# Kernel optimization log

Measured on AMD Instinct MI355X. Metric: run time of the kernel, lower is better.

Reference implementation:

```python
import math
import jax, jax.numpy as jnp
import numpy as np

B, S, D, H = 4, 1024, 1024, 16
DK = D // H
NEG = jnp.float32(-1e32)
EPS = 1e-5


def setup_inputs() -> dict:
    key = jax.random.key(0)
    ks = jax.random.split(key, 10)
    s = 1.0 / math.sqrt(D)
    return {
        "query": jax.random.normal(ks[0], (B, S, D), jnp.float32),
        "key": jax.random.normal(ks[1], (B, S, D), jnp.float32),
        "values": jax.random.normal(ks[2], (B, S, D), jnp.float32),
        "lens": jax.random.randint(ks[3], (B,), 0, S).astype(jnp.int32),
        "state_weight": jax.random.normal(ks[4], (1, H, S, S), jnp.float32),
        # params (kq_same=True -> k shares q_linear weights)
        "Wq": jax.random.normal(ks[5], (D, D), jnp.float32) * s,
        "bq": jnp.zeros((D,), jnp.float32),
        "Wv": jax.random.normal(ks[6], (D, D), jnp.float32) * s,
        "bv": jnp.zeros((D,), jnp.float32),
        "Wo": jax.random.normal(ks[7], (D, D), jnp.float32) * s,
        "bo": jnp.zeros((D,), jnp.float32),
        "gamma": jnp.ones((D,), jnp.float32),
        "beta": jnp.zeros((D,), jnp.float32),
    }


def reference(query, key, values, lens, state_weight, Wq, bq, Wv, bv, Wo, bo, gamma, beta):
    # eval-mode forward of DTransformerLayer (peek_cur=False -> strictly causal)
    b, s, d = query.shape
    mask = jnp.tril(jnp.ones((s, s), bool), -1)[None, None]  # [1,1,S,S]

    q = (query @ Wq + bq).reshape(b, s, H, DK).transpose(0, 2, 1, 3)   # bhsd
    k = (key @ Wq + bq).reshape(b, s, H, DK).transpose(0, 2, 1, 3)     # shared weights (kq_same)
    v = (values @ Wv + bv).reshape(b, s, H, DK).transpose(0, 2, 1, 3)

    scores = jnp.einsum('bhqd,bhkd->bhqk', q, k) / math.sqrt(DK)
    scores = jnp.where(mask, scores, NEG)
    scores = jnp.where(mask, scores + state_weight, NEG)
    attn = jax.nn.softmax(scores, axis=-1)
    attn = jnp.where(mask, attn, 0.0)  # fully-masked rows (row 0) -> zeros, matching torch

    ctx = jnp.einsum('bhqk,bhkd->bhqd', attn, v).transpose(0, 2, 1, 3).reshape(b, s, d)
    out = ctx @ Wo + bo

    x = query + out  # dropout is identity in eval
    mu = jnp.mean(x, axis=-1, keepdims=True)
    var = jnp.mean(jnp.square(x - mu), axis=-1, keepdims=True)
    return (x - mu) * jax.lax.rsqrt(var + EPS) * gamma + beta
```

## Files before the change

### kernel.cpp

```cpp
#include <hip/hip_runtime.h>

#define B_ 4
#define S_ 1024
#define D_ 1024
#define H_ 16
#define DK_ 64

typedef __attribute__((ext_vector_type(8))) short short8;
typedef __attribute__((ext_vector_type(4))) float f32x4;
typedef __attribute__((ext_vector_type(16))) float f32x16;

#define CBASE_PACK 0x100C090604020100ULL

static __device__ __forceinline__ unsigned bf16rne(float x) {
    unsigned b = __float_as_uint(x);
    return (b + 0x7FFFu + ((b >> 16) & 1u)) >> 16;
}

__global__ __launch_bounds__(256) void cvt3_bf16(
    const float* __restrict__ q, const float* __restrict__ k,
    const float* __restrict__ v, ushort* __restrict__ out)
{
    const size_t i = ((size_t)blockIdx.x * 256 + threadIdx.x) * 8;
    const size_t FM = (size_t)4 * 1024 * 1024;
    const float* in = (i < FM) ? q : (i < 2 * FM) ? k : v;
    const size_t off = i & (FM - 1);
    const float4 a = *reinterpret_cast<const float4*>(in + off);
    const float4 b = *reinterpret_cast<const float4*>(in + off + 4);
    union { ushort u[8]; int4 vv; } p;
    p.u[0] = (ushort)bf16rne(a.x); p.u[1] = (ushort)bf16rne(a.y);
    p.u[2] = (ushort)bf16rne(a.z); p.u[3] = (ushort)bf16rne(a.w);
    p.u[4] = (ushort)bf16rne(b.x); p.u[5] = (ushort)bf16rne(b.y);
    p.u[6] = (ushort)bf16rne(b.z); p.u[7] = (ushort)bf16rne(b.w);
    *reinterpret_cast<int4*>(out + i) = p.vv;
}

__global__ __launch_bounds__(256) void transpose_cvt3(
    const float* __restrict__ W0, const float* __restrict__ W1,
    const float* __restrict__ W2, ushort* __restrict__ T0,
    ushort* __restrict__ T1, ushort* __restrict__ T2)
{
    __shared__ float ts[32][33];
    const float* W = (blockIdx.z == 0) ? W0 : (blockIdx.z == 1) ? W1 : W2;
    ushort*     Wt = (blockIdx.z == 0) ? T0 : (blockIdx.z == 1) ? T1 : T2;
    const int t  = threadIdx.x;
    const int k0 = blockIdx.y * 32, n0 = blockIdx.x * 32;
    const int r  = t >> 3, c4 = (t & 7) * 4;
    const float4 v = *reinterpret_cast<const float4*>(&W[(size_t)(k0 + r) * 1024 + n0 + c4]);
    ts[r][c4] = v.x; ts[r][c4 + 1] = v.y; ts[r][c4 + 2] = v.z; ts[r][c4 + 3] = v.w;
    __syncthreads();
    ushort4 o;
    o.x = (ushort)bf16rne(ts[c4    ][r]);
    o.y = (ushort)bf16rne(ts[c4 + 1][r]);
    o.z = (ushort)bf16rne(ts[c4 + 2][r]);
    o.w = (ushort)bf16rne(ts[c4 + 3][r]);
    *reinterpret_cast<ushort4*>(&Wt[(size_t)(n0 + r) * 1024 + k0 + c4]) = o;
}

template<int MODE>
__global__ __launch_bounds__(256) void gemm_mfma(
    const ushort* __restrict__ X, const ushort* __restrict__ Wt,
    const float* __restrict__ bias, const float* __restrict__ resid,
    void* __restrict__ out0, void* __restrict__ out1)
{
    __shared__ ushort As[2][64 * 64];
    __shared__ ushort Bs[2][128 * 64];

    const int t    = threadIdx.x;
    const int lane = t & 63;
    const int w    = t >> 6;

    const int cpx     = gridDim.x >> 3;
    const int logical = (blockIdx.x & 7) * cpx + (blockIdx.x >> 3);
    const int bm = logical >> 3;
    const int bn = logical & 7;

    const int srow   = lane >> 3;
    const int schunk = (lane & 7) ^ srow;
    const ushort* ag[2];
    const ushort* bg[4];
#pragma unroll
    for (int j = 0; j < 2; ++j)
        ag[j] = X  + (size_t)(bm * 64 + (j * 4 + w) * 8 + srow) * 1024 + schunk * 8;
#pragma unroll
    for (int j = 0; j < 4; ++j)
        bg[j] = Wt + (size_t)(bn * 128 + (j * 4 + w) * 8 + srow) * 1024 + schunk * 8;

#define STAGE(buf, k0)                                                           \
    do {                                                                         \
        _Pragma("unroll")                                                        \
        for (int j = 0; j < 2; ++j)                                              \
            __builtin_amdgcn_global_load_lds(                                    \
                (__attribute__((address_space(1))) const void*)(ag[j] + (k0)),   \
                (__attribute__((address_space(3))) void*)&As[buf][(j * 4 + w) * 512], \
                16, 0, 0);                                                       \
        _Pragma("unroll")                                                        \
        for (int j = 0; j < 4; ++j)                                              \
            __builtin_amdgcn_global_load_lds(                                    \
                (__attribute__((address_space(1))) const void*)(bg[j] + (k0)),   \
                (__attribute__((address_space(3))) void*)&Bs[buf][(j * 4 + w) * 512], \
                16, 0, 0);                                                       \
    } while (0)

    const int fr = lane & 15;
    const int fk = lane >> 4;
    const int wm = w >> 1, wn = w & 1;

    f32x4 acc[2][4];
#pragma unroll
    for (int m = 0; m < 2; ++m)
#pragma unroll
        for (int n = 0; n < 4; ++n) acc[m][n] = (f32x4){0.f, 0.f, 0.f, 0.f};

    STAGE(0, 0);
#pragma unroll 1
    for (int kt = 0; kt < 16; ++kt) {
        const int cur = kt & 1;
        if (kt + 1 < 16) {
            STAGE(cur ^ 1, (kt + 1) * 64);
            asm volatile("s_waitcnt vmcnt(6)" ::: "memory");
        } else {
            asm volatile("s_waitcnt vmcnt(0)" ::: "memory");
        }
        __builtin_amdgcn_s_barrier();
        __builtin_amdgcn_sched_barrier(0);
#pragma unroll
        for (int ks = 0; ks < 2; ++ks) {
            short8 af[2], bf[4];
#pragma unroll
            for (int m = 0; m < 2; ++m) {
                const int row = wm * 32 + m * 16 + fr;
                af[m] = *reinterpret_cast<const short8*>(
                    &As[cur][row * 64 + (((ks * 4 + fk) ^ (row & 7)) * 8)]);
            }
#pragma unroll
            for (int n = 0; n < 4; ++n) {
                const int row = wn * 64 + n * 16 + fr;
                bf[n] = *reinterpret_cast<const short8*>(
                    &Bs[cur][row * 64 + (((ks * 4 + fk) ^ (row & 7)) * 8)]);
            }
            __builtin_amdgcn_s_setprio(1);
#pragma unroll
            for (int m = 0; m < 2; ++m)
#pragma unroll
                for (int n = 0; n < 4; ++n)
                    acc[m][n] = __builtin_amdgcn_mfma_f32_16x16x32_bf16(
                        af[m], bf[n], acc[m][n], 0, 0, 0);
            __builtin_amdgcn_s_setprio(0);
        }
        __builtin_amdgcn_sched_barrier(0);
        __builtin_amdgcn_s_barrier();
        __builtin_amdgcn_sched_barrier(0);
    }
#undef STAGE

#pragma unroll
    for (int m = 0; m < 2; ++m) {
        const int row0 = bm * 64 + wm * 32 + m * 16 + fk * 4;
#pragma unroll
        for (int n = 0; n < 4; ++n) {
            const int col = bn * 128 + wn * 64 + n * 16 + fr;
            const float bc = bias[col];
            if (MODE == 0) {
                float* o = (float*)out0;
#pragma unroll
                for (int j = 0; j < 4; ++j) {
                    const int row = row0 + j;
                    o[(size_t)row * 1024 + col] =
                        acc[m][n][j] + bc + resid[(size_t)row * 1024 + col];
                }
            } else if (MODE == 1) {
                ushort* o = (row0 < 4096) ? (ushort*)out0 : (ushort*)out1;
                const int r0 = row0 & 4095;
                const int b_ = r0 >> 10, s0 = r0 & 1023;
                const int h  = col >> 6,  dk = col & 63;
#pragma unroll
                for (int j = 0; j < 4; ++j)
                    o[(((size_t)b_ * H_ + h) * S_ + s0 + j) * DK_ + dk] =
                        (ushort)bf16rne(acc[m][n][j] + bc);
            } else {
                ushort* o = (ushort*)out0;
                const int b_ = row0 >> 10, s0 = row0 & 1023;
                const int h  = col >> 6,   dk = col & 63;
                ushort4 pk;
                pk.x = (ushort)bf16rne(acc[m][n][0] + bc);
                pk.y = (ushort)bf16rne(acc[m][n][1] + bc);
                pk.z = (ushort)bf16rne(acc[m][n][2] + bc);
                pk.w = (ushort)bf16rne(acc[m][n][3] + bc);
                *reinterpret_cast<ushort4*>(
                    &o[(((size_t)b_ * H_ + h) * DK_ + dk) * S_ + s0]) = pk;
            }
        }
    }
}

__global__ __launch_bounds__(256) void attn_mfma(
    const ushort* __restrict__ Qh, const ushort* __restrict__ Kh,
    const ushort* __restrict__ Vt, const float* __restrict__ SW,
    ushort* __restrict__ ctxP, float2* __restrict__ ml)
{
    __shared__ ushort Ks[2][4096];
    __shared__ ushort Vs[2][4096];

    const int t    = threadIdx.x;
    const int lane = t & 63;
    const int w    = t >> 6;
    const int lg = (blockIdx.x & 7) * 160 + (blockIdx.x >> 3);
    const int bh = lg / 20;
    const int ci = lg - bh * 20;
    const int b  = bh >> 4;
    const int h  = bh & 15;
    int qb = 0;
#pragma unroll
    for (int q = 1; q < 8; ++q)
        if ((int)((CBASE_PACK >> (q * 8)) & 0xff) <= ci) qb = q;
    const int lc = ci - (int)((CBASE_PACK >> (qb * 8)) & 0xff);
    const int t0 = lc * 4;
    const int nt = min(4, 2 * qb + 2 - t0);

    const int ql = lane & 31;
    const int hi = lane >> 5;
    const int qrow = qb * 128 + ql * 4 + w;

    const ushort* Kg  = Kh + (size_t)bh * S_ * DK_;
    const ushort* Vg  = Vt + (size_t)bh * DK_ * S_;
    const float*  swp = SW + ((size_t)h * S_ + qrow) * S_;

    const ushort* kgp[2];
    const ushort* vgp[2];
#pragma unroll
    for (int j = 0; j < 2; ++j) {
        const int bb = w * 2 + j;
        const int g = bb >> 2, c = bb & 3;
        kgp[j] = Kg + (size_t)(g * 32 + ql) * DK_ + c * 16 + hi * 8;
        vgp[j] = Vg + (size_t)(g * 32 + ql) * S_  + c * 16 + hi * 8;
    }

#define ASTAGE(buf, k0)                                                          \
    do {                                                                         \
        _Pragma("unroll")                                                        \
        for (int j = 0; j < 2; ++j) {                                            \
            const int bb = w * 2 + j;                                            \
            __builtin_amdgcn_global_load_lds(                                    \
                (__attribute__((address_space(1))) const void*)(kgp[j] + (size_t)(k0) * DK_), \
                (__attribute__((address_space(3))) void*)&Ks[buf][bb * 512],     \
                16, 0, 0);                                                       \
            __builtin_amdgcn_global_load_lds(                                    \
                (__attribute__((address_space(1))) const void*)(vgp[j] + (k0)),  \
                (__attribute__((address_space(3))) void*)&Vs[buf][bb * 512],     \
                16, 0, 0);                                                       \
        }                                                                        \
    } while (0)

    short8 qf[4];
    {
        const ushort* Qg = Qh + ((size_t)bh * S_ + qrow) * DK_;
#pragma unroll
        for (int c = 0; c < 4; ++c) {
            union { int4 i; short8 s; } u;
            u.i = *reinterpret_cast<const int4*>(&Qg[c * 16 + hi * 8]);
            qf[c] = u.s;
        }
    }

    f32x16 accA, accB;
#pragma unroll
    for (int r = 0; r < 16; ++r) { accA[r] = 0.f; accB[r] = 0.f; }
    float mrow = -1e30f, lrow = 0.f;

    ASTAGE(0, t0 * 64);

#pragma unroll 1
    for (int kt = 0; kt < nt; ++kt) {
        const int cur = kt & 1;
        const int k0  = (t0 + kt) * 64;
        if (kt + 1 < nt) {
            ASTAGE(cur ^ 1, (t0 + kt + 1) * 64);
            asm volatile("s_waitcnt vmcnt(4)" ::: "memory");
        } else {
            asm volatile("s_waitcnt vmcnt(0)" ::: "memory");
        }
        __builtin_amdgcn_s_barrier();
        __builtin_amdgcn_sched_barrier(0);

        f32x16 sc[2];
        __builtin_amdgcn_s_setprio(1);
#pragma unroll
        for (int g = 0; g < 2; ++g) {
#pragma unroll
            for (int r = 0; r < 16; ++r) sc[g][r] = 0.f;
#pragma unroll
            for (int c = 0; c < 4; ++c) {
                const short8 kf = *reinterpret_cast<const short8*>(
                    &Ks[cur][((g * 4 + c) * 64 + lane) * 8]);
                sc[g] = __builtin_amdgcn_mfma_f32_32x32x16_bf16(kf, qf[c], sc[g], 0, 0, 0);
            }
        }
        __builtin_amdgcn_s_setprio(0);

        float swv[2][16];
#pragma unroll
        for (int g = 0; g < 2; ++g)
#pragma unroll
            for (int j = 0; j < 4; ++j) {
                const float4 v = *reinterpret_cast<const float4*>(
                    &swp[k0 + g * 32 + hi * 4 + j * 8]);
                swv[g][j * 4 + 0] = v.x; swv[g][j * 4 + 1] = v.y;
                swv[g][j * 4 + 2] = v.z; swv[g][j * 4 + 3] = v.w;
            }

        float pr[2][16];
        float tmax = -1e30f;
        if (t0 + kt >= 2 * qb) {
#pragma unroll
            for (int g = 0; g < 2; ++g)
#pragma unroll
                for (int r = 0; r < 16; ++r) {
                    const int key = k0 + g * 32 + (r & 3) + ((r >> 2) << 3) + (hi << 2);
                    const float s = (key < qrow) ? sc[g][r] * 0.125f + swv[g][r] : -1e30f;
                    pr[g][r] = s;
                    tmax = fmaxf(tmax, s);
                }
        } else {
#pragma unroll
            for (int g = 0; g < 2; ++g)
#pragma unroll
                for (int r = 0; r < 16; ++r) {
                    const float s = sc[g][r] * 0.125f + swv[g][r];
                    pr[g][r] = s;
                    tmax = fmaxf(tmax, s);
                }
        }
        tmax = fmaxf(tmax, __shfl_xor(tmax, 32, 64));
        const float mnew = fmaxf(mrow, tmax);
        const float corr = __expf(mrow - mnew);
        float psum = 0.f;
#pragma unroll
        for (int g = 0; g < 2; ++g)
#pragma unroll
            for (int r = 0; r < 16; ++r) {
                const float e = (pr[g][r] > -1e29f) ? __expf(pr[g][r] - mnew) : 0.f;
                pr[g][r] = e;
                psum += e;
            }
        psum += __shfl_xor(psum, 32, 64);
        lrow = lrow * corr + psum;
        mrow = mnew;
#pragma unroll
        for (int r = 0; r < 16; ++r) { accA[r] *= corr; accB[r] *= corr; }

        short8 paf[4];
#pragma unroll
        for (int g = 0; g < 2; ++g) {
            unsigned pk[8];
#pragma unroll
            for (int j = 0; j < 8; ++j) {
                unsigned r_;
                asm("v_cvt_pk_bf16_f32 %0, %1, %2"
                    : "=v"(r_) : "v"(pr[g][2 * j]), "v"(pr[g][2 * j + 1]));
                pk[j] = r_;
            }
            unsigned x0 = (unsigned)__shfl_xor((int)pk[0], 32, 64);
            unsigned x1 = (unsigned)__shfl_xor((int)pk[1], 32, 64);
            unsigned x2 = (unsigned)__shfl_xor((int)pk[2], 32, 64);
            unsigned x3 = (unsigned)__shfl_xor((int)pk[3], 32, 64);
            unsigned x4 = (unsigned)__shfl_xor((int)pk[4], 32, 64);
            unsigned x5 = (unsigned)__shfl_xor((int)pk[5], 32, 64);
            unsigned x6 = (unsigned)__shfl_xor((int)pk[6], 32, 64);
            unsigned x7 = (unsigned)__shfl_xor((int)pk[7], 32, 64);
            union { unsigned u[4]; short8 s; } a0, a1;
            a0.u[0] = hi ? x2 : pk[0];
            a0.u[1] = hi ? x3 : pk[1];
            a0.u[2] = hi ? pk[2] : x0;
            a0.u[3] = hi ? pk[3] : x1;
            a1.u[0] = hi ? x6 : pk[4];
            a1.u[1] = hi ? x7 : pk[5];
            a1.u[2] = hi ? pk[6] : x4;
            a1.u[3] = hi ? pk[7] : x5;
            paf[g * 2 + 0] = a0.s;
            paf[g * 2 + 1] = a1.s;
        }

        __builtin_amdgcn_s_setprio(1);
#pragma unroll
        for (int cc = 0; cc < 4; ++cc) {
            const short8 va = *reinterpret_cast<const short8*>(
                &Vs[cur][((0 * 4 + cc) * 64 + lane) * 8]);
            const short8 vb = *reinterpret_cast<const short8*>(
                &Vs[cur][((1 * 4 + cc) * 64 + lane) * 8]);
            accA = __builtin_amdgcn_mfma_f32_32x32x16_bf16(va, paf[cc], accA, 0, 0, 0);
            accB = __builtin_amdgcn_mfma_f32_32x32x16_bf16(vb, paf[cc], accB, 0, 0, 0);
        }
        __builtin_amdgcn_s_setprio(0);

        __builtin_amdgcn_sched_barrier(0);
        __builtin_amdgcn_s_barrier();
        __builtin_amdgcn_sched_barrier(0);
    }
#undef ASTAGE

    const float inv = (lrow > 0.f) ? 1.f / lrow : 0.f;
    ushort* crow_ = ctxP + ((size_t)(bh * 20 + ci) * 128 + (ql * 4 + w)) * 64;
#pragma unroll
    for (int g = 0; g < 4; ++g) {
        ushort4 oA, oB;
        oA.x = (ushort)bf16rne(accA[4 * g + 0] * inv);
        oA.y = (ushort)bf16rne(accA[4 * g + 1] * inv);
        oA.z = (ushort)bf16rne(accA[4 * g + 2] * inv);
        oA.w = (ushort)bf16rne(accA[4 * g + 3] * inv);
        oB.x = (ushort)bf16rne(accB[4 * g + 0] * inv);
        oB.y = (ushort)bf16rne(accB[4 * g + 1] * inv);
        oB.z = (ushort)bf16rne(accB[4 * g + 2] * inv);
        oB.w = (ushort)bf16rne(accB[4 * g + 3] * inv);
        *reinterpret_cast<ushort4*>(&crow_[g * 8 + hi * 4])      = oA;
        *reinterpret_cast<ushort4*>(&crow_[g * 8 + hi * 4 + 32]) = oB;
    }
    if (hi == 0) {
        float2 v; v.x = mrow; v.y = lrow;
        ml[(size_t)(bh * 20 + ci) * 128 + ql * 4 + w] = v;
    }
}

__global__ __launch_bounds__(256) void attn_merge(
    const ushort* __restrict__ ctxP, const float2* __restrict__ ml,
    ushort* __restrict__ ctx)
{
    const size_t idx = ((size_t)blockIdx.x * 256 + threadIdx.x) * 8;
    const int col = (int)(idx & 1023);
    const int row = (int)(idx >> 10);
    const int b = row >> 10, s = row & 1023;
    const int h = col >> 6, dk0 = col & 63;
    const int bh = b * 16 + h;
    const int qb = s >> 7, rl = s & 127;
    const int nch = (qb + 2) >> 1;
    const int cb  = (int)((CBASE_PACK >> (qb * 8)) & 0xff);

    float mm[4], ll[4];
    float m = -1e30f;
#pragma unroll
    for (int c = 0; c < 4; ++c)
        if (c < nch) {
            const float2 v = ml[(size_t)(bh * 20 + cb + c) * 128 + rl];
            mm[c] = v.x; ll[c] = v.y;
            m = fmaxf(m, v.x);
        }
    float wc[4], wsum = 0.f;
#pragma unroll
    for (int c = 0; c < 4; ++c)
        if (c < nch) { wc[c] = ll[c] * __expf(mm[c] - m); wsum += wc[c]; }
    const float inv = (wsum > 0.f) ? 1.f / wsum : 0.f;

    float o[8] = {0.f, 0.f, 0.f, 0.f, 0.f, 0.f, 0.f, 0.f};
#pragma unroll
    for (int c = 0; c < 4; ++c)
        if (c < nch) {
            union { int4 v; ushort u[8]; } p;
            p.v = *reinterpret_cast<const int4*>(
                &ctxP[((size_t)(bh * 20 + cb + c) * 128 + rl) * 64 + dk0]);
            const float wgt = wc[c] * inv;
#pragma unroll
            for (int i = 0; i < 8; ++i)
                o[i] += wgt * __uint_as_float((unsigned)p.u[i] << 16);
        }
    union { int4 v; ushort u[8]; } r;
#pragma unroll
    for (int i = 0; i < 8; ++i) r.u[i] = (ushort)bf16rne(o[i]);
    *reinterpret_cast<int4*>(ctx + idx) = r.v;
}

__global__ __launch_bounds__(256) void layernorm_k(
    const float* __restrict__ x, const float* __restrict__ gamma,
    const float* __restrict__ beta, float* __restrict__ out)
{
    const int row = blockIdx.x;
    const int t   = threadIdx.x;
    const float4 v = *reinterpret_cast<const float4*>(&x[(size_t)row * D_ + (t << 2)]);
    float sum = v.x + v.y + v.z + v.w;
    float sq  = v.x * v.x + v.y * v.y + v.z * v.z + v.w * v.w;
#pragma unroll
    for (int w = 1; w < 64; w <<= 1) {
        sum += __shfl_xor(sum, w, 64);
        sq  += __shfl_xor(sq,  w, 64);
    }
    __shared__ float red[8];
    const int wid = t >> 6;
    if ((t & 63) == 0) { red[wid] = sum; red[wid + 4] = sq; }
    __syncthreads();
    sum = red[0] + red[1] + red[2] + red[3];
    sq  = red[4] + red[5] + red[6] + red[7];
    const float mu  = sum * (1.f / 1024.f);
    const float var = sq * (1.f / 1024.f) - mu * mu;
    const float rs  = rsqrtf(var + 1e-5f);
    const float4 gm = *reinterpret_cast<const float4*>(&gamma[t << 2]);
    const float4 bt = *reinterpret_cast<const float4*>(&beta[t << 2]);
    float4 o;
    o.x = (v.x - mu) * rs * gm.x + bt.x;
    o.y = (v.y - mu) * rs * gm.y + bt.y;
    o.z = (v.z - mu) * rs * gm.z + bt.z;
    o.w = (v.w - mu) * rs * gm.w + bt.w;
    *reinterpret_cast<float4*>(&out[(size_t)row * D_ + (t << 2)]) = o;
}

extern "C" void kernel_launch(void* const* d_in, const int* in_sizes, int n_in,
                              void* d_out, int out_size, void* d_ws, size_t ws_size,
                              hipStream_t stream)
{
    const float* query  = (const float*)d_in[0];
    const float* key    = (const float*)d_in[1];
    const float* values = (const float*)d_in[2];
    const float* SW     = (const float*)d_in[4];
    const float* Wq     = (const float*)d_in[5];
    const float* bq     = (const float*)d_in[6];
    const float* Wv     = (const float*)d_in[7];
    const float* bv     = (const float*)d_in[8];
    const float* Wo     = (const float*)d_in[9];
    const float* bo     = (const float*)d_in[10];
    const float* gamma  = (const float*)d_in[11];
    const float* beta   = (const float*)d_in[12];

    char* ws = (char*)d_ws;
    const size_t MB = 1024 * 1024;
    ushort* Qh   = (ushort*)(ws);
    ushort* Kh   = (ushort*)(ws +  8 * MB);
    ushort* Vt   = (ushort*)(ws + 16 * MB);
    ushort* Wqt  = (ushort*)(ws + 24 * MB);
    ushort* Wvt  = (ushort*)(ws + 26 * MB);
    ushort* Wot  = (ushort*)(ws + 28 * MB);
    ushort* qbf  = (ushort*)(ws + 30 * MB);
    ushort* kbf  = (ushort*)(ws + 38 * MB);
    ushort* vbf  = (ushort*)(ws + 46 * MB);
    float2* ml   = (float2*)(ws + 54 * MB);
    ushort* ctxP = qbf;
    ushort* ctxm = Qh;
    float*  xbf  = (float*)(ws + 8 * MB);

    const dim3 blk(256);

    cvt3_bf16<<<dim3(6144), blk, 0, stream>>>(query, key, values, qbf);
    transpose_cvt3<<<dim3(32, 32, 3), blk, 0, stream>>>(Wq, Wv, Wo, Wqt, Wvt, Wot);

    gemm_mfma<1><<<dim3(1024), blk, 0, stream>>>(qbf, Wqt, bq, nullptr, Qh, Kh);
    gemm_mfma<2><<<dim3(512),  blk, 0, stream>>>(vbf, Wvt, bv, nullptr, Vt, nullptr);

    attn_mfma<<<dim3(1280), blk, 0, stream>>>(Qh, Kh, Vt, SW, ctxP, ml);
    attn_merge<<<dim3(2048), blk, 0, stream>>>(ctxP, ml, ctxm);

    gemm_mfma<0><<<dim3(512), blk, 0, stream>>>(ctxm, Wot, bo, query, xbf, nullptr);

    layernorm_k<<<dim3(4096), blk, 0, stream>>>(xbf, gamma, beta, (float*)d_out);
}
```

Baseline: 148.1 us.

## Prefetch state_weight tiles in registers, fold Q scaling into projection, remap blocks

Moves the state_weight loads out of the softmax critical path by double-buffering them in registers one tile ahead, alongside the existing K/V LDS staging. The loop is unrolled by two so buffer indices are static. The 1/sqrt(dk) scale is folded into the Q projection epilogue, and the unmasked exp path drops its mask compare. The block-to-(b,h,chunk) mapping now interleaves batches so concurrent blocks share state_weight rows in cache, and launch bounds request 3 blocks per CU. The register prefetch raises VGPR pressure. The unrolled loop assumes an even tile count nt, and runs tile kt+1 even when nt is odd.

Result: slower. 234.4 us (+58.3%).

```diff
diff --git a/kernel.cpp b/kernel.cpp
--- a/kernel.cpp
+++ b/kernel.cpp
@@ -171,13 +171,14 @@
                 }
             } else if (MODE == 1) {
                 ushort* o = (row0 < 4096) ? (ushort*)out0 : (ushort*)out1;
+                const float qs = (row0 < 4096) ? 0.125f : 1.0f;
                 const int r0 = row0 & 4095;
                 const int b_ = r0 >> 10, s0 = r0 & 1023;
                 const int h  = col >> 6,  dk = col & 63;
 #pragma unroll
                 for (int j = 0; j < 4; ++j)
                     o[(((size_t)b_ * H_ + h) * S_ + s0 + j) * DK_ + dk] =
-                        (ushort)bf16rne(acc[m][n][j] + bc);
+                        (ushort)bf16rne((acc[m][n][j] + bc) * qs);
             } else {
                 ushort* o = (ushort*)out0;
                 const int b_ = row0 >> 10, s0 = row0 & 1023;
@@ -194,7 +195,7 @@
     }
 }
 
-__global__ __launch_bounds__(256) void attn_mfma(
+__global__ __launch_bounds__(256, 3) void attn_mfma(
     const ushort* __restrict__ Qh, const ushort* __restrict__ Kh,
     const ushort* __restrict__ Vt, const float* __restrict__ SW,
     ushort* __restrict__ ctxP, float2* __restrict__ ml)
@@ -206,10 +207,11 @@
     const int lane = t & 63;
     const int w    = t >> 6;
     const int lg = (blockIdx.x & 7) * 160 + (blockIdx.x >> 3);
-    const int bh = lg / 20;
-    const int ci = lg - bh * 20;
-    const int b  = bh >> 4;
-    const int h  = bh & 15;
+    const int b  = lg & 3;
+    const int hc = lg >> 2;
+    const int h  = hc / 20;
+    const int ci = hc % 20;
+    const int bh = b * 16 + h;
     int qb = 0;
 #pragma unroll
     for (int q = 1; q < 8; ++q)
@@ -252,6 +254,16 @@
         }                                                                        \
     } while (0)
 
+#define SWLOAD(dst, k0)                                                          \
+    do {                                                                         \
+        _Pragma("unroll")                                                        \
+        for (int g2 = 0; g2 < 2; ++g2)                                           \
+            _Pragma("unroll")                                                    \
+            for (int j2 = 0; j2 < 4; ++j2)                                       \
+                dst[g2 * 4 + j2] = *reinterpret_cast<const float4*>(             \
+                    &swp[(k0) + g2 * 32 + hi * 4 + j2 * 8]);                     \
+    } while (0)
+
     short8 qf[4];
     {
         const ushort* Qg = Qh + ((size_t)bh * S_ + qrow) * DK_;
@@ -268,18 +280,10 @@
     for (int r = 0; r < 16; ++r) { accA[r] = 0.f; accB[r] = 0.f; }
     float mrow = -1e30f, lrow = 0.f;
 
-    ASTAGE(0, t0 * 64);
-
-#pragma unroll 1
-    for (int kt = 0; kt < nt; ++kt) {
-        const int cur = kt & 1;
-        const int k0  = (t0 + kt) * 64;
-        if (kt + 1 < nt) {
-            ASTAGE(cur ^ 1, (t0 + kt + 1) * 64);
-            asm volatile("s_waitcnt vmcnt(4)" ::: "memory");
-        } else {
-            asm volatile("s_waitcnt vmcnt(0)" ::: "memory");
-        }
+    float4 swA[8], swB[8];
+
+    auto tile_body = [&](int ktt, int cur, const float4 (&swc)[8]) {
+        const int k0 = (t0 + ktt) * 64;
         __builtin_amdgcn_s_barrier();
         __builtin_amdgcn_sched_barrier(0);
 
@@ -298,27 +302,17 @@
         }
         __builtin_amdgcn_s_setprio(0);
 
-        float swv[2][16];
-#pragma unroll
-        for (int g = 0; g < 2; ++g)
-#pragma unroll
-            for (int j = 0; j < 4; ++j) {
-                const float4 v = *reinterpret_cast<const float4*>(
-                    &swp[k0 + g * 32 + hi * 4 + j * 8]);
-                swv[g][j * 4 + 0] = v.x; swv[g][j * 4 + 1] = v.y;
-                swv[g][j * 4 + 2] = v.z; swv[g][j * 4 + 3] = v.w;
-            }
-
-        float pr[2][16];
+        const bool masked = (t0 + ktt >= 2 * qb);
         float tmax = -1e30f;
-        if (t0 + kt >= 2 * qb) {
+        if (masked) {
 #pragma unroll
             for (int g = 0; g < 2; ++g)
 #pragma unroll
                 for (int r = 0; r < 16; ++r) {
                     const int key = k0 + g * 32 + (r & 3) + ((r >> 2) << 3) + (hi << 2);
-                    const float s = (key < qrow) ? sc[g][r] * 0.125f + swv[g][r] : -1e30f;
-                    pr[g][r] = s;
+                    const float swv = ((const float*)&swc[g * 4 + (r >> 2)])[r & 3];
+                    const float s = (key < qrow) ? sc[g][r] + swv : -1e30f;
+                    sc[g][r] = s;
                     tmax = fmaxf(tmax, s);
                 }
         } else {
@@ -326,8 +320,9 @@
             for (int g = 0; g < 2; ++g)
 #pragma unroll
                 for (int r = 0; r < 16; ++r) {
-                    const float s = sc[g][r] * 0.125f + swv[g][r];
-                    pr[g][r] = s;
+                    const float swv = ((const float*)&swc[g * 4 + (r >> 2)])[r & 3];
+                    const float s = sc[g][r] + swv;
+                    sc[g][r] = s;
                     tmax = fmaxf(tmax, s);
                 }
         }
@@ -335,14 +330,25 @@
         const float mnew = fmaxf(mrow, tmax);
         const float corr = __expf(mrow - mnew);
         float psum = 0.f;
-#pragma unroll
-        for (int g = 0; g < 2; ++g)
-#pragma unroll
-            for (int r = 0; r < 16; ++r) {
-                const float e = (pr[g][r] > -1e29f) ? __expf(pr[g][r] - mnew) : 0.f;
-                pr[g][r] = e;
-                psum += e;
-            }
+        if (masked) {
+#pragma unroll
+            for (int g = 0; g < 2; ++g)
+#pragma unroll
+                for (int r = 0; r < 16; ++r) {
+                    const float e = (sc[g][r] > -1e29f) ? __expf(sc[g][r] - mnew) : 0.f;
+                    sc[g][r] = e;
+                    psum += e;
+                }
+        } else {
+#pragma unroll
+            for (int g = 0; g < 2; ++g)
+#pragma unroll
+                for (int r = 0; r < 16; ++r) {
+                    const float e = __expf(sc[g][r] - mnew);
+                    sc[g][r] = e;
+                    psum += e;
+                }
+        }
         psum += __shfl_xor(psum, 32, 64);
         lrow = lrow * corr + psum;
         mrow = mnew;
@@ -357,7 +363,7 @@
             for (int j = 0; j < 8; ++j) {
                 unsigned r_;
                 asm("v_cvt_pk_bf16_f32 %0, %1, %2"
-                    : "=v"(r_) : "v"(pr[g][2 * j]), "v"(pr[g][2 * j + 1]));
+                    : "=v"(r_) : "v"(sc[g][2 * j]), "v"(sc[g][2 * j + 1]));
                 pk[j] = r_;
             }
             unsigned x0 = (unsigned)__shfl_xor((int)pk[0], 32, 64);
@@ -396,8 +402,29 @@
         __builtin_amdgcn_sched_barrier(0);
         __builtin_amdgcn_s_barrier();
         __builtin_amdgcn_sched_barrier(0);
+    };
+
+    SWLOAD(swA, t0 * 64);
+    ASTAGE(0, t0 * 64);
+
+#pragma unroll 1
+    for (int kt = 0; kt < nt; kt += 2) {
+        SWLOAD(swB, (t0 + kt + 1) * 64);
+        ASTAGE(1, (t0 + kt + 1) * 64);
+        asm volatile("s_waitcnt vmcnt(12)" ::: "memory");
+        tile_body(kt, 0, swA);
+
+        if (kt + 2 < nt) {
+            SWLOAD(swA, (t0 + kt + 2) * 64);
+            ASTAGE(0, (t0 + kt + 2) * 64);
+            asm volatile("s_waitcnt vmcnt(12)" ::: "memory");
+        } else {
+            asm volatile("s_waitcnt vmcnt(0)" ::: "memory");
+        }
+        tile_body(kt + 1, 1, swB);
     }
 #undef ASTAGE
+#undef SWLOAD
 
     const float inv = (lrow > 0.f) ? 1.f / lrow : 0.f;
     ushort* crow_ = ctxP + ((size_t)(bh * 20 + ci) * 128 + (ql * 4 + w)) * 64;
```

## Drop LDS staging in attention, load K/V to registers, fold scale and bias

Applied to the files above, without the earlier changes.

The attention kernel no longer double-buffers K/V tiles through shared memory with block barriers. Each wave now loads its K and V fragments straight from global memory into registers and prefetches the next K tile and state_weight tile. The 1/sqrt(dk) scale moves into the Q projection epilogue, and state_weight seeds the score MFMA accumulator, removing the per-element scale and add. Block indexing is remapped so the four batches sharing a head's state_weight rows run next to each other, aiming for better L2 reuse. In exchange, all four waves now fetch the same K/V fragments separately, which multiplies global/L2 traffic and raises register pressure.

Result: slower. 165.9 us (+12.0%).

```diff
diff --git a/kernel.cpp b/kernel.cpp
--- a/kernel.cpp
+++ b/kernel.cpp
@@ -171,13 +171,14 @@
                 }
             } else if (MODE == 1) {
                 ushort* o = (row0 < 4096) ? (ushort*)out0 : (ushort*)out1;
+                const float qs = (row0 < 4096) ? 0.125f : 1.0f;
                 const int r0 = row0 & 4095;
                 const int b_ = r0 >> 10, s0 = r0 & 1023;
                 const int h  = col >> 6,  dk = col & 63;
 #pragma unroll
                 for (int j = 0; j < 4; ++j)
                     o[(((size_t)b_ * H_ + h) * S_ + s0 + j) * DK_ + dk] =
-                        (ushort)bf16rne(acc[m][n][j] + bc);
+                        (ushort)bf16rne((acc[m][n][j] + bc) * qs);
             } else {
                 ushort* o = (ushort*)out0;
                 const int b_ = row0 >> 10, s0 = row0 & 1023;
@@ -199,17 +200,15 @@
     const ushort* __restrict__ Vt, const float* __restrict__ SW,
     ushort* __restrict__ ctxP, float2* __restrict__ ml)
 {
-    __shared__ ushort Ks[2][4096];
-    __shared__ ushort Vs[2][4096];
-
     const int t    = threadIdx.x;
     const int lane = t & 63;
     const int w    = t >> 6;
     const int lg = (blockIdx.x & 7) * 160 + (blockIdx.x >> 3);
-    const int bh = lg / 20;
-    const int ci = lg - bh * 20;
-    const int b  = bh >> 4;
-    const int h  = bh & 15;
+    const int b  = lg & 3;
+    const int hc = lg >> 2;
+    const int h  = hc / 20;
+    const int ci = hc % 20;
+    const int bh = b * 16 + h;
     int qb = 0;
 #pragma unroll
     for (int q = 1; q < 8; ++q)
@@ -226,32 +225,6 @@
     const ushort* Vg  = Vt + (size_t)bh * DK_ * S_;
     const float*  swp = SW + ((size_t)h * S_ + qrow) * S_;
 
-    const ushort* kgp[2];
-    const ushort* vgp[2];
-#pragma unroll
-    for (int j = 0; j < 2; ++j) {
-        const int bb = w * 2 + j;
-        const int g = bb >> 2, c = bb & 3;
-        kgp[j] = Kg + (size_t)(g * 32 + ql) * DK_ + c * 16 + hi * 8;
-        vgp[j] = Vg + (size_t)(g * 32 + ql) * S_  + c * 16 + hi * 8;
-    }
-
-#define ASTAGE(buf, k0)                                                          \
-    do {                                                                         \
-        _Pragma("unroll")                                                        \
-        for (int j = 0; j < 2; ++j) {                                            \
-            const int bb = w * 2 + j;                                            \
-            __builtin_amdgcn_global_load_lds(                                    \
-                (__attribute__((address_space(1))) const void*)(kgp[j] + (size_t)(k0) * DK_), \
-                (__attribute__((address_space(3))) void*)&Ks[buf][bb * 512],     \
-                16, 0, 0);                                                       \
-            __builtin_amdgcn_global_load_lds(                                    \
-                (__attribute__((address_space(1))) const void*)(vgp[j] + (k0)),  \
-                (__attribute__((address_space(3))) void*)&Vs[buf][bb * 512],     \
-                16, 0, 0);                                                       \
-        }                                                                        \
-    } while (0)
-
     short8 qf[4];
     {
         const ushort* Qg = Qh + ((size_t)bh * S_ + qrow) * DK_;
@@ -268,136 +241,142 @@
     for (int r = 0; r < 16; ++r) { accA[r] = 0.f; accB[r] = 0.f; }
     float mrow = -1e30f, lrow = 0.f;
 
-    ASTAGE(0, t0 * 64);
-
+    int4 kA[8];
+    int4 vv[8];
+    float4 sA[8], sB[8];
+
+#define LOADK(kt_)                                                               \
+    do {                                                                         \
+        const size_t kb_ = (size_t)(t0 + (kt_)) * 64 * DK_;                      \
+        _Pragma("unroll")                                                        \
+        for (int j = 0; j < 8; ++j)                                              \
+            kA[j] = *reinterpret_cast<const int4*>(                              \
+                &Kg[kb_ + (size_t)((j >> 2) * 32 + ql) * DK_ + (j & 3) * 16 + hi * 8]); \
+    } while (0)
+
+#define LOADV(kt_)                                                               \
+    do {                                                                         \
+        const int kv_ = (t0 + (kt_)) * 64;                                       \
+        _Pragma("unroll")                                                        \
+        for (int j = 0; j < 8; ++j)                                              \
+            vv[j] = *reinterpret_cast<const int4*>(                              \
+                &Vg[(size_t)((j >> 2) * 32 + ql) * S_ + kv_ + (j & 3) * 16 + hi * 8]); \
+    } while (0)
+
+#define LOADS(dst, kt_)                                                          \
+    do {                                                                         \
+        const int ks_ = (t0 + (kt_)) * 64;                                       \
+        _Pragma("unroll")                                                        \
+        for (int j = 0; j < 8; ++j)                                              \
+            dst[j] = *reinterpret_cast<const float4*>(                           \
+                &swp[ks_ + (j >> 2) * 32 + hi * 4 + (j & 3) * 8]);               \
+    } while (0)
+
+#define BODY(CURS, NXTS, ktt)                                                    \
+    do {                                                                         \
+        const int k0_ = (t0 + (ktt)) * 64;                                       \
+        LOADV(ktt);                                                              \
+                            \
+        f32x16 sc0, sc1;                                                         \
+        _Pragma("unroll")                                                        \
+        for (int r = 0; r < 16; ++r) {                                           \
+            sc0[r] = ((const float*)&CURS[(r >> 2)])[r & 3];                     \
+            sc1[r] = ((const float*)&CURS[4 + (r >> 2)])[r & 3];                 \
+        }                                                                        \
+        _Pragma("unroll")                                                        \
+        for (int c = 0; c < 4; ++c) {                                            \
+            union { int4 i; short8 s; } k0u, k1u;                                \
+            k0u.i = kA[c];  k1u.i = kA[4 + c];                                   \
+            sc0 = __builtin_amdgcn_mfma_f32_32x32x16_bf16(k0u.s, qf[c], sc0, 0, 0, 0); \
+            sc1 = __builtin_amdgcn_mfma_f32_32x32x16_bf16(k1u.s, qf[c], sc1, 0, 0, 0); \
+        }                                                                        \
+                           \
+        if ((ktt) + 1 < nt) { LOADK((ktt) + 1); LOADS(NXTS, (ktt) + 1); }        \
+                                \
+        float tmax = -1e30f;                                                     \
+        if (t0 + (ktt) >= 2 * qb) {                                              \
+            _Pragma("unroll")                                                    \
+            for (int r = 0; r < 16; ++r) {                                       \
+                const int key0 = k0_ + (r & 3) + ((r >> 2) << 3) + (hi << 2);    \
+                if (key0 >= qrow)      sc0[r] = -1e30f;                          \
+                if (key0 + 32 >= qrow) sc1[r] = -1e30f;                          \
+                tmax = fmaxf(tmax, fmaxf(sc0[r], sc1[r]));                       \
+            }                                                                    \
+        } else {                                                                 \
+            _Pragma("unroll")                                                    \
+            for (int r = 0; r < 16; ++r)                                         \
+                tmax = fmaxf(tmax, fmaxf(sc0[r], sc1[r]));                       \
+        }                                                                        \
+        tmax = fmaxf(tmax, __shfl_xor(tmax, 32, 64));                            \
+        const float mnew = fmaxf(mrow, tmax);                                    \
+        const float corr = __expf(mrow - mnew);                                  \
+        float psum = 0.f;                                                        \
+        _Pragma("unroll")                                                        \
+        for (int r = 0; r < 16; ++r) {                                           \
+            const float e0 = (sc0[r] > -1e29f) ? __expf(sc0[r] - mnew) : 0.f;    \
+            const float e1 = (sc1[r] > -1e29f) ? __expf(sc1[r] - mnew) : 0.f;    \
+            sc0[r] = e0; sc1[r] = e1;                                            \
+            psum += e0 + e1;                                                     \
+        }                                                                        \
+        psum += __shfl_xor(psum, 32, 64);                                        \
+        lrow = lrow * corr + psum;                                               \
+        mrow = mnew;                                                             \
+        _Pragma("unroll")                                                        \
+        for (int r = 0; r < 16; ++r) { accA[r] *= corr; accB[r] *= corr; }       \
+                       \
+        short8 paf[4];                                                           \
+        _Pragma("unroll")                                                        \
+        for (int g = 0; g < 2; ++g) {                                            \
+            unsigned pk[8];                                                      \
+            _Pragma("unroll")                                                    \
+            for (int j = 0; j < 8; ++j) {                                        \
+                unsigned r_;                                                     \
+                const float lo_ = g ? sc1[2 * j]     : sc0[2 * j];               \
+                const float hi_ = g ? sc1[2 * j + 1] : sc0[2 * j + 1];           \
+                asm("v_cvt_pk_bf16_f32 %0, %1, %2" : "=v"(r_) : "v"(lo_), "v"(hi_)); \
+                pk[j] = r_;                                                      \
+            }                                                                    \
+            unsigned x0 = (unsigned)__shfl_xor((int)pk[0], 32, 64);              \
+            unsigned x1 = (unsigned)__shfl_xor((int)pk[1], 32, 64);              \
+            unsigned x2 = (unsigned)__shfl_xor((int)pk[2], 32, 64);              \
+            unsigned x3 = (unsigned)__shfl_xor((int)pk[3], 32, 64);              \
+            unsigned x4 = (unsigned)__shfl_xor((int)pk[4], 32, 64);              \
+            unsigned x5 = (unsigned)__shfl_xor((int)pk[5], 32, 64);              \
+            unsigned x6 = (unsigned)__shfl_xor((int)pk[6], 32, 64);              \
+            unsigned x7 = (unsigned)__shfl_xor((int)pk[7], 32, 64);              \
+            union { unsigned u[4]; short8 s; } a0, a1;                           \
+            a0.u[0] = hi ? x2 : pk[0];                                           \
+            a0.u[1] = hi ? x3 : pk[1];                                           \
+            a0.u[2] = hi ? pk[2] : x0;                                           \
+            a0.u[3] = hi ? pk[3] : x1;                                           \
+            a1.u[0] = hi ? x6 : pk[4];                                           \
+            a1.u[1] = hi ? x7 : pk[5];                                           \
+            a1.u[2] = hi ? pk[6] : x4;                                           \
+            a1.u[3] = hi ? pk[7] : x5;                                           \
+            paf[g * 2 + 0] = a0.s;                                               \
+            paf[g * 2 + 1] = a1.s;                                               \
+        }                                                                        \
+                                             \
+        _Pragma("unroll")                                                        \
+        for (int cc = 0; cc < 4; ++cc) {                                         \
+            union { int4 i; short8 s; } va, vb;                                  \
+            va.i = vv[cc]; vb.i = vv[4 + cc];                                    \
+            accA = __builtin_amdgcn_mfma_f32_32x32x16_bf16(va.s, paf[cc], accA, 0, 0, 0); \
+            accB = __builtin_amdgcn_mfma_f32_32x32x16_bf16(vb.s, paf[cc], accB, 0, 0, 0); \
+        }                                                                        \
+    } while (0)
+
+    LOADK(0);
+    LOADS(sA, 0);
 #pragma unroll 1
-    for (int kt = 0; kt < nt; ++kt) {
-        const int cur = kt & 1;
-        const int k0  = (t0 + kt) * 64;
-        if (kt + 1 < nt) {
-            ASTAGE(cur ^ 1, (t0 + kt + 1) * 64);
-            asm volatile("s_waitcnt vmcnt(4)" ::: "memory");
-        } else {
-            asm volatile("s_waitcnt vmcnt(0)" ::: "memory");
-        }
-        __builtin_amdgcn_s_barrier();
-        __builtin_amdgcn_sched_barrier(0);
-
-        f32x16 sc[2];
-        __builtin_amdgcn_s_setprio(1);
-#pragma unroll
-        for (int g = 0; g < 2; ++g) {
-#pragma unroll
-            for (int r = 0; r < 16; ++r) sc[g][r] = 0.f;
-#pragma unroll
-            for (int c = 0; c < 4; ++c) {
-                const short8 kf = *reinterpret_cast<const short8*>(
-                    &Ks[cur][((g * 4 + c) * 64 + lane) * 8]);
-                sc[g] = __builtin_amdgcn_mfma_f32_32x32x16_bf16(kf, qf[c], sc[g], 0, 0, 0);
-            }
-        }
-        __builtin_amdgcn_s_setprio(0);
-
-        float swv[2][16];
-#pragma unroll
-        for (int g = 0; g < 2; ++g)
-#pragma unroll
-            for (int j = 0; j < 4; ++j) {
-                const float4 v = *reinterpret_cast<const float4*>(
-                    &swp[k0 + g * 32 + hi * 4 + j * 8]);
-                swv[g][j * 4 + 0] = v.x; swv[g][j * 4 + 1] = v.y;
-                swv[g][j * 4 + 2] = v.z; swv[g][j * 4 + 3] = v.w;
-            }
-
-        float pr[2][16];
-        float tmax = -1e30f;
-        if (t0 + kt >= 2 * qb) {
-#pragma unroll
-            for (int g = 0; g < 2; ++g)
-#pragma unroll
-                for (int r = 0; r < 16; ++r) {
-                    const int key = k0 + g * 32 + (r & 3) + ((r >> 2) << 3) + (hi << 2);
-                    const float s = (key < qrow) ? sc[g][r] * 0.125f + swv[g][r] : -1e30f;
-                    pr[g][r] = s;
-                    tmax = fmaxf(tmax, s);
-                }
-        } else {
-#pragma unroll
-            for (int g = 0; g < 2; ++g)
-#pragma unroll
-                for (int r = 0; r < 16; ++r) {
-                    const float s = sc[g][r] * 0.125f + swv[g][r];
-                    pr[g][r] = s;
-                    tmax = fmaxf(tmax, s);
-                }
-        }
-        tmax = fmaxf(tmax, __shfl_xor(tmax, 32, 64));
-        const float mnew = fmaxf(mrow, tmax);
-        const float corr = __expf(mrow - mnew);
-        float psum = 0.f;
-#pragma unroll
-        for (int g = 0; g < 2; ++g)
-#pragma unroll
-            for (int r = 0; r < 16; ++r) {
-                const float e = (pr[g][r] > -1e29f) ? __expf(pr[g][r] - mnew) : 0.f;
-                pr[g][r] = e;
-                psum += e;
-            }
-        psum += __shfl_xor(psum, 32, 64);
-        lrow = lrow * corr + psum;
-        mrow = mnew;
-#pragma unroll
-        for (int r = 0; r < 16; ++r) { accA[r] *= corr; accB[r] *= corr; }
-
-        short8 paf[4];
-#pragma unroll
-        for (int g = 0; g < 2; ++g) {
-            unsigned pk[8];
-#pragma unroll
-            for (int j = 0; j < 8; ++j) {
-                unsigned r_;
-                asm("v_cvt_pk_bf16_f32 %0, %1, %2"
-                    : "=v"(r_) : "v"(pr[g][2 * j]), "v"(pr[g][2 * j + 1]));
-                pk[j] = r_;
-            }
-            unsigned x0 = (unsigned)__shfl_xor((int)pk[0], 32, 64);
-            unsigned x1 = (unsigned)__shfl_xor((int)pk[1], 32, 64);
-            unsigned x2 = (unsigned)__shfl_xor((int)pk[2], 32, 64);
-            unsigned x3 = (unsigned)__shfl_xor((int)pk[3], 32, 64);
-            unsigned x4 = (unsigned)__shfl_xor((int)pk[4], 32, 64);
-            unsigned x5 = (unsigned)__shfl_xor((int)pk[5], 32, 64);
-            unsigned x6 = (unsigned)__shfl_xor((int)pk[6], 32, 64);
-            unsigned x7 = (unsigned)__shfl_xor((int)pk[7], 32, 64);
-            union { unsigned u[4]; short8 s; } a0, a1;
-            a0.u[0] = hi ? x2 : pk[0];
-            a0.u[1] = hi ? x3 : pk[1];
-            a0.u[2] = hi ? pk[2] : x0;
-            a0.u[3] = hi ? pk[3] : x1;
-            a1.u[0] = hi ? x6 : pk[4];
-            a1.u[1] = hi ? x7 : pk[5];
-            a1.u[2] = hi ? pk[6] : x4;
-            a1.u[3] = hi ? pk[7] : x5;
-            paf[g * 2 + 0] = a0.s;
-            paf[g * 2 + 1] = a1.s;
-        }
-
-        __builtin_amdgcn_s_setprio(1);
-#pragma unroll
-        for (int cc = 0; cc < 4; ++cc) {
-            const short8 va = *reinterpret_cast<const short8*>(
-                &Vs[cur][((0 * 4 + cc) * 64 + lane) * 8]);
-            const short8 vb = *reinterpret_cast<const short8*>(
-                &Vs[cur][((1 * 4 + cc) * 64 + lane) * 8]);
-            accA = __builtin_amdgcn_mfma_f32_32x32x16_bf16(va, paf[cc], accA, 0, 0, 0);
-            accB = __builtin_amdgcn_mfma_f32_32x32x16_bf16(vb, paf[cc], accB, 0, 0, 0);
-        }
-        __builtin_amdgcn_s_setprio(0);
-
-        __builtin_amdgcn_sched_barrier(0);
-        __builtin_amdgcn_s_barrier();
-        __builtin_amdgcn_sched_barrier(0);
-    }
-#undef ASTAGE
+    for (int kt = 0; kt < nt; kt += 2) {
+        BODY(sA, sB, kt);
+        BODY(sB, sA, kt + 1);
+    }
+#undef LOADK
+#undef LOADV
+#undef LOADS
+#undef BODY
 
     const float inv = (lrow > 0.f) ? 1.f / lrow : 0.f;
     ushort* crow_ = ctxP + ((size_t)(bh * 20 + ci) * 128 + (ql * 4 + w)) * 64;
```

## Fuse fp32-to-bf16 input conversion into projection GEMMs and fold score scale into Q

Applied to the files above, without the earlier changes.

Removes the separate cvt3_bf16 pass. The projection GEMMs now load fp32 activations into registers, convert them with v_cvt_pk_bf16_f32 and write bf16 to LDS, while B still goes through direct global-to-LDS loads. The 1/sqrt(dk) scale is applied to Q in the GEMM epilogue, so the attention kernel no longer multiplies scores. The attention kernel also reorders its block-to-(batch, head) mapping and issues the state_weight loads before the QK MFMAs to hide their latency. The cost is that the GEMM A loads go through registers with a conversion step, which adds register pressure and waitcnt bookkeeping in the main loop.

New measurement: 145.0 us. 2.1% less time.

```diff
diff --git a/kernel.cpp b/kernel.cpp
--- a/kernel.cpp
+++ b/kernel.cpp
@@ -15,24 +15,6 @@
 static __device__ __forceinline__ unsigned bf16rne(float x) {
     unsigned b = __float_as_uint(x);
     return (b + 0x7FFFu + ((b >> 16) & 1u)) >> 16;
-}
-
-__global__ __launch_bounds__(256) void cvt3_bf16(
-    const float* __restrict__ q, const float* __restrict__ k,
-    const float* __restrict__ v, ushort* __restrict__ out)
-{
-    const size_t i = ((size_t)blockIdx.x * 256 + threadIdx.x) * 8;
-    const size_t FM = (size_t)4 * 1024 * 1024;
-    const float* in = (i < FM) ? q : (i < 2 * FM) ? k : v;
-    const size_t off = i & (FM - 1);
-    const float4 a = *reinterpret_cast<const float4*>(in + off);
-    const float4 b = *reinterpret_cast<const float4*>(in + off + 4);
-    union { ushort u[8]; int4 vv; } p;
-    p.u[0] = (ushort)bf16rne(a.x); p.u[1] = (ushort)bf16rne(a.y);
-    p.u[2] = (ushort)bf16rne(a.z); p.u[3] = (ushort)bf16rne(a.w);
-    p.u[4] = (ushort)bf16rne(b.x); p.u[5] = (ushort)bf16rne(b.y);
-    p.u[6] = (ushort)bf16rne(b.z); p.u[7] = (ushort)bf16rne(b.w);
-    *reinterpret_cast<int4*>(out + i) = p.vv;
 }
 
 __global__ __launch_bounds__(256) void transpose_cvt3(
@@ -58,10 +40,175 @@
 }
 
 template<int MODE>
-__global__ __launch_bounds__(256) void gemm_mfma(
+__global__ __launch_bounds__(256) void gemm_f32a(
+    const float* __restrict__ Xf0, const float* __restrict__ Xf1,
+    const ushort* __restrict__ Wt, const float* __restrict__ bias,
+    void* __restrict__ out0, void* __restrict__ out1)
+{
+    __shared__ ushort As[2][64 * 64];
+    __shared__ ushort Bs[2][128 * 64];
+
+    const int t    = threadIdx.x;
+    const int lane = t & 63;
+    const int w    = t >> 6;
+
+    const int cpx     = gridDim.x >> 3;
+    const int logical = (blockIdx.x & 7) * cpx + (blockIdx.x >> 3);
+    const int bm = logical >> 3;
+    const int bn = logical & 7;
+
+    const int srow   = lane >> 3;
+    const int schunk = (lane & 7) ^ srow;
+
+    const float* Xf = (MODE == 1 && bm >= 64) ? Xf1 : Xf0;
+    const int rbase = (bm * 64) & 4095;
+    const float* ap[2];
+#pragma unroll
+    for (int j = 0; j < 2; ++j)
+        ap[j] = Xf + (size_t)(rbase + (j * 4 + w) * 8 + srow) * 1024 + schunk * 8;
+
+    const ushort* bg[4];
+#pragma unroll
+    for (int j = 0; j < 4; ++j)
+        bg[j] = Wt + (size_t)(bn * 128 + (j * 4 + w) * 8 + srow) * 1024 + schunk * 8;
+
+    float4 aRx0, aRy0, aRx1, aRy1;
+
+#define A_ISSUE(k0)                                                              \
+    do {                                                                         \
+        aRx0 = *reinterpret_cast<const float4*>(ap[0] + (k0));                   \
+        aRy0 = *reinterpret_cast<const float4*>(ap[0] + (k0) + 4);               \
+        aRx1 = *reinterpret_cast<const float4*>(ap[1] + (k0));                   \
+        aRy1 = *reinterpret_cast<const float4*>(ap[1] + (k0) + 4);               \
+    } while (0)
+
+#define B_STAGE(buf, k0)                                                         \
+    do {                                                                         \
+        _Pragma("unroll")                                                        \
+        for (int j = 0; j < 4; ++j)                                              \
+            __builtin_amdgcn_global_load_lds(                                    \
+                (__attribute__((address_space(1))) const void*)(bg[j] + (k0)),   \
+                (__attribute__((address_space(3))) void*)&Bs[buf][(j * 4 + w) * 512], \
+                16, 0, 0);                                                       \
+    } while (0)
+
+#define A_WRITE(buf)                                                             \
+    do {                                                                         \
+        union { unsigned u[4]; int4 v; } p0, p1;                                 \
+        asm("v_cvt_pk_bf16_f32 %0, %1, %2" : "=v"(p0.u[0]) : "v"(aRx0.x), "v"(aRx0.y)); \
+        asm("v_cvt_pk_bf16_f32 %0, %1, %2" : "=v"(p0.u[1]) : "v"(aRx0.z), "v"(aRx0.w)); \
+        asm("v_cvt_pk_bf16_f32 %0, %1, %2" : "=v"(p0.u[2]) : "v"(aRy0.x), "v"(aRy0.y)); \
+        asm("v_cvt_pk_bf16_f32 %0, %1, %2" : "=v"(p0.u[3]) : "v"(aRy0.z), "v"(aRy0.w)); \
+        asm("v_cvt_pk_bf16_f32 %0, %1, %2" : "=v"(p1.u[0]) : "v"(aRx1.x), "v"(aRx1.y)); \
+        asm("v_cvt_pk_bf16_f32 %0, %1, %2" : "=v"(p1.u[1]) : "v"(aRx1.z), "v"(aRx1.w)); \
+        asm("v_cvt_pk_bf16_f32 %0, %1, %2" : "=v"(p1.u[2]) : "v"(aRy1.x), "v"(aRy1.y)); \
+        asm("v_cvt_pk_bf16_f32 %0, %1, %2" : "=v"(p1.u[3]) : "v"(aRy1.z), "v"(aRy1.w)); \
+        *reinterpret_cast<int4*>(&As[buf][((0 * 4 + w) * 64 + lane) * 8]) = p0.v; \
+        *reinterpret_cast<int4*>(&As[buf][((1 * 4 + w) * 64 + lane) * 8]) = p1.v; \
+    } while (0)
+
+    const int fr = lane & 15;
+    const int fk = lane >> 4;
+    const int wm = w >> 1, wn = w & 1;
+
+    f32x4 acc[2][4];
+#pragma unroll
+    for (int m = 0; m < 2; ++m)
+#pragma unroll
+        for (int n = 0; n < 4; ++n) acc[m][n] = (f32x4){0.f, 0.f, 0.f, 0.f};
+
+    A_ISSUE(0);
+    B_STAGE(0, 0);
+    asm volatile("s_waitcnt vmcnt(4)" ::: "memory");
+    A_WRITE(0);
+    asm volatile("s_waitcnt lgkmcnt(0)" ::: "memory");
+
+#pragma unroll 1
+    for (int kt = 0; kt < 16; ++kt) {
+        const int cur = kt & 1;
+        if (kt + 1 < 16) {
+            A_ISSUE((kt + 1) * 64);
+            B_STAGE(cur ^ 1, (kt + 1) * 64);
+            asm volatile("s_waitcnt vmcnt(8)" ::: "memory");
+        } else {
+            asm volatile("s_waitcnt vmcnt(0)" ::: "memory");
+        }
+        __builtin_amdgcn_s_barrier();
+        __builtin_amdgcn_sched_barrier(0);
+#pragma unroll
+        for (int ks = 0; ks < 2; ++ks) {
+            short8 af[2], bf[4];
+#pragma unroll
+            for (int m = 0; m < 2; ++m) {
+                const int row = wm * 32 + m * 16 + fr;
+                af[m] = *reinterpret_cast<const short8*>(
+                    &As[cur][row * 64 + (((ks * 4 + fk) ^ (row & 7)) * 8)]);
+            }
+#pragma unroll
+            for (int n = 0; n < 4; ++n) {
+                const int row = wn * 64 + n * 16 + fr;
+                bf[n] = *reinterpret_cast<const short8*>(
+                    &Bs[cur][row * 64 + (((ks * 4 + fk) ^ (row & 7)) * 8)]);
+            }
+            __builtin_amdgcn_s_setprio(1);
+#pragma unroll
+            for (int m = 0; m < 2; ++m)
+#pragma unroll
+                for (int n = 0; n < 4; ++n)
+                    acc[m][n] = __builtin_amdgcn_mfma_f32_16x16x32_bf16(
+                        af[m], bf[n], acc[m][n], 0, 0, 0);
+            __builtin_amdgcn_s_setprio(0);
+        }
+        if (kt + 1 < 16) {
+            asm volatile("s_waitcnt vmcnt(4)" ::: "memory");
+            A_WRITE(cur ^ 1);
+            asm volatile("s_waitcnt lgkmcnt(0)" ::: "memory");
+        }
+        __builtin_amdgcn_sched_barrier(0);
+        __builtin_amdgcn_s_barrier();
+        __builtin_amdgcn_sched_barrier(0);
+    }
+#undef A_ISSUE
+#undef B_STAGE
+#undef A_WRITE
+
+#pragma unroll
+    for (int m = 0; m < 2; ++m) {
+        const int row0 = bm * 64 + wm * 32 + m * 16 + fk * 4;
+#pragma unroll
+        for (int n = 0; n < 4; ++n) {
+            const int col = bn * 128 + wn * 64 + n * 16 + fr;
+            const float bc = bias[col];
+            if (MODE == 1) {
+                ushort* o = (row0 < 4096) ? (ushort*)out0 : (ushort*)out1;
+                const float qs = (row0 < 4096) ? 0.125f : 1.0f;
+                const int r0 = row0 & 4095;
+                const int b_ = r0 >> 10, s0 = r0 & 1023;
+                const int h  = col >> 6,  dk = col & 63;
+#pragma unroll
+                for (int j = 0; j < 4; ++j)
+                    o[(((size_t)b_ * H_ + h) * S_ + s0 + j) * DK_ + dk] =
+                        (ushort)bf16rne((acc[m][n][j] + bc) * qs);
+            } else {
+                ushort* o = (ushort*)out0;
+                const int b_ = row0 >> 10, s0 = row0 & 1023;
+                const int h  = col >> 6,   dk = col & 63;
+                ushort4 pk;
+                pk.x = (ushort)bf16rne(acc[m][n][0] + bc);
+                pk.y = (ushort)bf16rne(acc[m][n][1] + bc);
+                pk.z = (ushort)bf16rne(acc[m][n][2] + bc);
+                pk.w = (ushort)bf16rne(acc[m][n][3] + bc);
+                *reinterpret_cast<ushort4*>(
+                    &o[(((size_t)b_ * H_ + h) * DK_ + dk) * S_ + s0]) = pk;
+            }
+        }
+    }
+}
+
+__global__ __launch_bounds__(256) void gemm_bf16a(
     const ushort* __restrict__ X, const ushort* __restrict__ Wt,
     const float* __restrict__ bias, const float* __restrict__ resid,
-    void* __restrict__ out0, void* __restrict__ out1)
+    float* __restrict__ out)
 {
     __shared__ ushort As[2][64 * 64];
     __shared__ ushort Bs[2][128 * 64];
@@ -161,34 +308,11 @@
         for (int n = 0; n < 4; ++n) {
             const int col = bn * 128 + wn * 64 + n * 16 + fr;
             const float bc = bias[col];
-            if (MODE == 0) {
-                float* o = (float*)out0;
-#pragma unroll
-                for (int j = 0; j < 4; ++j) {
-                    const int row = row0 + j;
-                    o[(size_t)row * 1024 + col] =
-                        acc[m][n][j] + bc + resid[(size_t)row * 1024 + col];
-                }
-            } else if (MODE == 1) {
-                ushort* o = (row0 < 4096) ? (ushort*)out0 : (ushort*)out1;
-                const int r0 = row0 & 4095;
-                const int b_ = r0 >> 10, s0 = r0 & 1023;
-                const int h  = col >> 6,  dk = col & 63;
-#pragma unroll
-                for (int j = 0; j < 4; ++j)
-                    o[(((size_t)b_ * H_ + h) * S_ + s0 + j) * DK_ + dk] =
-                        (ushort)bf16rne(acc[m][n][j] + bc);
-            } else {
-                ushort* o = (ushort*)out0;
-                const int b_ = row0 >> 10, s0 = row0 & 1023;
-                const int h  = col >> 6,   dk = col & 63;
-                ushort4 pk;
-                pk.x = (ushort)bf16rne(acc[m][n][0] + bc);
-                pk.y = (ushort)bf16rne(acc[m][n][1] + bc);
-                pk.z = (ushort)bf16rne(acc[m][n][2] + bc);
-                pk.w = (ushort)bf16rne(acc[m][n][3] + bc);
-                *reinterpret_cast<ushort4*>(
-                    &o[(((size_t)b_ * H_ + h) * DK_ + dk) * S_ + s0]) = pk;
+#pragma unroll
+            for (int j = 0; j < 4; ++j) {
+                const int row = row0 + j;
+                out[(size_t)row * 1024 + col] =
+                    acc[m][n][j] + bc + resid[(size_t)row * 1024 + col];
             }
         }
     }
@@ -206,10 +330,11 @@
     const int lane = t & 63;
     const int w    = t >> 6;
     const int lg = (blockIdx.x & 7) * 160 + (blockIdx.x >> 3);
-    const int bh = lg / 20;
-    const int ci = lg - bh * 20;
-    const int b  = bh >> 4;
-    const int h  = bh & 15;
+    const int b  = lg & 3;
+    const int hc = lg >> 2;
+    const int h  = hc / 20;
+    const int ci = hc % 20;
+    const int bh = b * 16 + h;
     int qb = 0;
 #pragma unroll
     for (int q = 1; q < 8; ++q)
@@ -283,21 +408,6 @@
         __builtin_amdgcn_s_barrier();
         __builtin_amdgcn_sched_barrier(0);
 
-        f32x16 sc[2];
-        __builtin_amdgcn_s_setprio(1);
-#pragma unroll
-        for (int g = 0; g < 2; ++g) {
-#pragma unroll
-            for (int r = 0; r < 16; ++r) sc[g][r] = 0.f;
-#pragma unroll
-            for (int c = 0; c < 4; ++c) {
-                const short8 kf = *reinterpret_cast<const short8*>(
-                    &Ks[cur][((g * 4 + c) * 64 + lane) * 8]);
-                sc[g] = __builtin_amdgcn_mfma_f32_32x32x16_bf16(kf, qf[c], sc[g], 0, 0, 0);
-            }
-        }
-        __builtin_amdgcn_s_setprio(0);
-
         float swv[2][16];
 #pragma unroll
         for (int g = 0; g < 2; ++g)
@@ -309,6 +419,21 @@
                 swv[g][j * 4 + 2] = v.z; swv[g][j * 4 + 3] = v.w;
             }
 
+        f32x16 sc[2];
+        __builtin_amdgcn_s_setprio(1);
+#pragma unroll
+        for (int g = 0; g < 2; ++g) {
+#pragma unroll
+            for (int r = 0; r < 16; ++r) sc[g][r] = 0.f;
+#pragma unroll
+            for (int c = 0; c < 4; ++c) {
+                const short8 kf = *reinterpret_cast<const short8*>(
+                    &Ks[cur][((g * 4 + c) * 64 + lane) * 8]);
+                sc[g] = __builtin_amdgcn_mfma_f32_32x32x16_bf16(kf, qf[c], sc[g], 0, 0, 0);
+            }
+        }
+        __builtin_amdgcn_s_setprio(0);
+
         float pr[2][16];
         float tmax = -1e30f;
         if (t0 + kt >= 2 * qb) {
@@ -317,7 +442,7 @@
 #pragma unroll
                 for (int r = 0; r < 16; ++r) {
                     const int key = k0 + g * 32 + (r & 3) + ((r >> 2) << 3) + (hi << 2);
-                    const float s = (key < qrow) ? sc[g][r] * 0.125f + swv[g][r] : -1e30f;
+                    const float s = (key < qrow) ? sc[g][r] + swv[g][r] : -1e30f;
                     pr[g][r] = s;
                     tmax = fmaxf(tmax, s);
                 }
@@ -326,7 +451,7 @@
             for (int g = 0; g < 2; ++g)
 #pragma unroll
                 for (int r = 0; r < 16; ++r) {
-                    const float s = sc[g][r] * 0.125f + swv[g][r];
+                    const float s = sc[g][r] + swv[g][r];
                     pr[g][r] = s;
                     tmax = fmaxf(tmax, s);
                 }
@@ -526,26 +651,22 @@
     ushort* Wqt  = (ushort*)(ws + 24 * MB);
     ushort* Wvt  = (ushort*)(ws + 26 * MB);
     ushort* Wot  = (ushort*)(ws + 28 * MB);
-    ushort* qbf  = (ushort*)(ws + 30 * MB);
-    ushort* kbf  = (ushort*)(ws + 38 * MB);
-    ushort* vbf  = (ushort*)(ws + 46 * MB);
-    float2* ml   = (float2*)(ws + 54 * MB);
-    ushort* ctxP = qbf;
+    ushort* ctxP = (ushort*)(ws + 30 * MB);
+    float2* ml   = (float2*)(ws + 52 * MB);
     ushort* ctxm = Qh;
     float*  xbf  = (float*)(ws + 8 * MB);
 
     const dim3 blk(256);
 
-    cvt3_bf16<<<dim3(6144), blk, 0, stream>>>(query, key, values, qbf);
     transpose_cvt3<<<dim3(32, 32, 3), blk, 0, stream>>>(Wq, Wv, Wo, Wqt, Wvt, Wot);
 
-    gemm_mfma<1><<<dim3(1024), blk, 0, stream>>>(qbf, Wqt, bq, nullptr, Qh, Kh);
-    gemm_mfma<2><<<dim3(512),  blk, 0, stream>>>(vbf, Wvt, bv, nullptr, Vt, nullptr);
+    gemm_f32a<1><<<dim3(1024), blk, 0, stream>>>(query, key, Wqt, bq, Qh, Kh);
+    gemm_f32a<2><<<dim3(512),  blk, 0, stream>>>(values, nullptr, Wvt, bv, Vt, nullptr);
 
     attn_mfma<<<dim3(1280), blk, 0, stream>>>(Qh, Kh, Vt, SW, ctxP, ml);
     attn_merge<<<dim3(2048), blk, 0, stream>>>(ctxP, ml, ctxm);
 
-    gemm_mfma<0><<<dim3(512), blk, 0, stream>>>(ctxm, Wot, bo, query, xbf, nullptr);
+    gemm_bf16a<<<dim3(512), blk, 0, stream>>>(ctxm, Wot, bo, query, xbf);
 
     layernorm_k<<<dim3(4096), blk, 0, stream>>>(xbf, gamma, beta, (float*)d_out);
 }
```
